# Optimization experiments

Hardware: AMD Instinct MI355X
Metric: run time of the kernel (lower is better)

The kernel has to match this reference:

```python
import jax, jax.numpy as jnp
import numpy as np
from jax import lax

H = 65  # hidden size

def lstm_layer(x, w_ih, w_hh, b_ih, b_hh):
    # x: [B, T, in]; w_ih: [4H, in]; w_hh: [4H, H]; PyTorch gate order i,f,g,o
    B = x.shape[0]
    # precompute input contribution for all timesteps: [T, B, 4H]
    pre = jnp.einsum('bti,gi->tbg', x, w_ih) + (b_ih + b_hh)
    wh = w_hh.T  # [H, 4H]

    def step(carry, pre_t):
        h, c = carry
        gates = pre_t + h @ wh
        i, f, g, o = jnp.split(gates, 4, axis=-1)
        i = jax.nn.sigmoid(i)
        f = jax.nn.sigmoid(f)
        g = jnp.tanh(g)
        o = jax.nn.sigmoid(o)
        c = f * c + i * g
        h = o * jnp.tanh(c)
        return (h, c), h

    init = (jnp.zeros((B, H), x.dtype), jnp.zeros((B, H), x.dtype))
    _, hs = lax.scan(step, init, pre)  # hs: [T, B, H]
    return jnp.transpose(hs, (1, 0, 2))  # [B, T, H]


def setup_inputs() -> dict:
    key = jax.random.key(0)
    ks = jax.random.split(key, 11)
    B, T = 512, 1024
    s = 1.0 / np.sqrt(H)
    d = {
        'x': jax.random.normal(ks[0], (B, T, H), jnp.float32),
        'w_ih0': jax.random.normal(ks[1], (4 * H, H), jnp.float32) * s,
        'w_hh0': jax.random.normal(ks[2], (4 * H, H), jnp.float32) * s,
        'b_ih0': jax.random.normal(ks[3], (4 * H,), jnp.float32) * s,
        'b_hh0': jax.random.normal(ks[4], (4 * H,), jnp.float32) * s,
        'w_ih1': jax.random.normal(ks[5], (4 * H, H), jnp.float32) * s,
        'w_hh1': jax.random.normal(ks[6], (4 * H, H), jnp.float32) * s,
        'b_ih1': jax.random.normal(ks[7], (4 * H,), jnp.float32) * s,
        'b_hh1': jax.random.normal(ks[8], (4 * H,), jnp.float32) * s,
        'w_lin': jax.random.normal(ks[9], (1, H), jnp.float32) * s,
        'b_lin': jax.random.normal(ks[10], (1,), jnp.float32) * s,
    }
    return d


def reference(x, w_ih0, w_hh0, b_ih0, b_hh0, w_ih1, w_hh1, b_ih1, b_hh1, w_lin, b_lin):
    h1 = lstm_layer(x, w_ih0, w_hh0, b_ih0, b_hh0)   # [B, T, H]
    h2 = lstm_layer(h1, w_ih1, w_hh1, b_ih1, b_hh1)  # [B, T, H]
    last = h2[:, -1, :]                               # [B, H]
    return last @ w_lin.T + b_lin                     # [B, 1]
```

## Files before the change

### kernel.cpp

```cpp
#include <hip/hip_runtime.h>

#define H 65
#define T_STEPS 1024

typedef _Float16 half_t;
typedef _Float16 half2_t __attribute__((ext_vector_type(2)));

static __device__ __forceinline__ float dot2(half2_t a, half2_t b, float c) {
#if __has_builtin(__builtin_amdgcn_fdot2)
  return __builtin_amdgcn_fdot2(a, b, c, false);
#else
  float d;
  asm("v_dot2_f32_f16 %0, %1, %2, %3" : "=v"(d) : "v"(a), "v"(b), "v"(c));
  return d;
#endif
}

template <int CTRL>
static __device__ __forceinline__ float qperm(float v) {
  int r = __builtin_amdgcn_update_dpp(0, __builtin_bit_cast(int, v), CTRL, 0xF, 0xF, true);
  return __builtin_bit_cast(float, r);
}

template <int PAT>
static __device__ __forceinline__ float swz(float v) {
  int r = __builtin_amdgcn_ds_swizzle(__builtin_bit_cast(int, v), PAT);
  return __builtin_bit_cast(float, r);
}

#define LOG2E 1.44269504089f
static __device__ __forceinline__ float fast_sigm(float v) {
  float e = __builtin_amdgcn_exp2f(-LOG2E * v);
  return __builtin_amdgcn_rcpf(1.f + e);
}

static __device__ __forceinline__ float pick(int idx, float a, float b, float c, float d) {
  float lo = (idx & 1) ? b : a;
  float hi = (idx & 1) ? d : c;
  return (idx & 2) ? hi : lo;
}

__global__ __launch_bounds__(512, 4) void lstm_fused(
    const float* __restrict__ x,
    const float* __restrict__ wih0, const float* __restrict__ whh0,
    const float* __restrict__ bih0, const float* __restrict__ bhh0,
    const float* __restrict__ wih1, const float* __restrict__ whh1,
    const float* __restrict__ bih1, const float* __restrict__ bhh1,
    const float* __restrict__ wlin, const float* __restrict__ blin,
    float* __restrict__ out)
{
  __shared__ __align__(16) half_t xh[2][2][144];
  __shared__ float h1f[H];

  const int tid = threadIdx.x;
  const int b   = blockIdx.x;

  const int quad = tid >> 2;
  const int l  = (quad >= 65) ? 1 : 0;
  const int j  = quad - 65 * l;
  const int kh = (tid >> 1) & 1;
  const int g0 = tid & 1;
  const bool gz = (g0 == 0);
  const float mreg = gz ? 2.f : 1.f;
  const float msub = mreg - 1.f;

  half2_t w[2][33];
  float hb[2];
  {
    const float* wi = l ? wih1 : wih0;
    const float* wh = l ? whh1 : whh0;
    const float* bi = l ? bih1 : bih0;
    const float* bh = l ? bhh1 : bhh0;
#pragma unroll
    for (int cc = 0; cc < 2; ++cc) {
      const int row = (g0 + 2 * cc) * H + j;
      hb[cc] = 0.5f * (bi[row] + bh[row]);
      const float* src = (kh ? wh : wi) + row * H;
#pragma unroll
      for (int pp = 0; pp < 33; ++pp) {
        float e0 = src[2 * pp];
        float e1 = (2 * pp + 1 < H) ? src[2 * pp + 1] : 0.f;
        half2_t v = {(half_t)e0, (half_t)e1};
        w[cc][pp] = v;
      }
    }
  }

  const bool isW7 = (tid >= 448);
  const int  w7   = tid - 448;
  const int  ec   = w7 >> 3;
  const int  ck   = w7 & 7;
  const int  side = ck >> 2;
  const int  sck  = ck & 3;
  const int  ecoff = side * 144 + 36 * sck;
  half2_t ecw[9];
  float ecbias = 0.f;
  float cec = 0.f;
  if (isW7) {
    const int gec = ec & 3;
    const int jec = 63 + (ec >> 2);
    const int row = gec * H + jec;
    const float* src = (side ? whh1 : wih1) + row * H;
#pragma unroll
    for (int i = 0; i < 9; ++i) {
      int es = 9 * sck + i;
      float e0 = (es < 33) ? src[2 * es] : 0.f;
      float e1 = (es < 33 && 2 * es + 1 < H) ? src[2 * es + 1] : 0.f;
      half2_t v = {(half_t)e0, (half_t)e1};
      ecw[i] = v;
    }
    if (ck == 0) ecbias = bih1[row] + bhh1[row];
  } else {
#pragma unroll
    for (int i = 0; i < 9; ++i) {
      half2_t z = {(half_t)0.f, (half_t)0.f};
      ecw[i] = z;
    }
  }

  const bool isW6 = (tid >= 384) && (tid < 448);
  const int  u    = tid - 384;

  for (int i = tid; i < 2 * 2 * 144; i += 512) ((half_t*)xh)[i] = (half_t)0.f;
  __syncthreads();

  const float* xrow = x + (size_t)b * (size_t)(T_STEPS * H);
  float nxA = 0.f, nxB = 0.f, nnA = 0.f, nnB = 0.f;
  if (isW6) {
    xh[0][0][u] = (half_t)xrow[u];
    if (u == 0) xh[0][0][64] = (half_t)xrow[64];
    nxA = xrow[H + u];
    if (u == 0) nxB = xrow[H + 64];
    nnA = xrow[2 * H + u];
    if (u == 0) nnB = xrow[2 * H + 64];
  }
  __syncthreads();

  float cst = 0.f;

  for (int s = 0; s <= T_STEPS; ++s) {
    const int p = s & 1;

    float fA = 0.f, fB = 0.f;
    if (isW6 && (s + 3 < T_STEPS)) {
      const float* xr = xrow + (size_t)(s + 3) * H;
      fA = xr[u];
      if (u == 0) fB = xr[64];
    }

    const bool act = l ? (s >= 1) : (s < T_STEPS);
    if (act) {
      const half_t* xb = &xh[l][p][0] + 72 * kh;
      float a0 = hb[0], a1 = hb[1];
#pragma unroll
      for (int c = 0; c < 8; ++c) {
        uint4 qv = ((const uint4*)xb)[c];
        half2_t x0 = __builtin_bit_cast(half2_t, qv.x);
        half2_t x1 = __builtin_bit_cast(half2_t, qv.y);
        half2_t x2 = __builtin_bit_cast(half2_t, qv.z);
        half2_t x3 = __builtin_bit_cast(half2_t, qv.w);
        a0 = dot2(x0, w[0][4 * c + 0], a0);
        a1 = dot2(x0, w[1][4 * c + 0], a1);
        a0 = dot2(x1, w[0][4 * c + 1], a0);
        a1 = dot2(x1, w[1][4 * c + 1], a1);
        a0 = dot2(x2, w[0][4 * c + 2], a0);
        a1 = dot2(x2, w[1][4 * c + 2], a1);
        a0 = dot2(x3, w[0][4 * c + 3], a0);
        a1 = dot2(x3, w[1][4 * c + 3], a1);
      }
      {
        half2_t xt = *(const half2_t*)(xb + 64);
        a0 = dot2(xt, w[0][32], a0);
        a1 = dot2(xt, w[1][32], a1);
      }
      a0 += qperm<0x4E>(a0);
      a1 += qperm<0x4E>(a1);
      float e0 = fast_sigm(a0);
      float e1 = mreg * fast_sigm(mreg * a1) - msub;
      float p0 = qperm<0xB1>(e0);
      float p1 = qperm<0xB1>(e1);
      float iv = gz ? e0 : p0;
      float fv = gz ? p0 : e0;
      float gv = gz ? e1 : p1;
      float ov = gz ? p1 : e1;
      cst = fv * cst + iv * gv;
      float th = 2.f * fast_sigm(2.f * cst) - 1.f;
      float hv = ov * th;
      if ((tid & 3) == 0) {
        half_t hh = (half_t)hv;
        if (l == 0) {
          xh[0][p ^ 1][72 + j] = hh;
          xh[1][p ^ 1][j]      = hh;
        } else {
          xh[1][p ^ 1][72 + j] = hh;
          if (s == T_STEPS) h1f[j] = hv;
        }
      }
    }

    if (isW7 && s >= 1) {
      const char* xb1 = (const char*)&xh[1][p][0];
      float aec = ecbias;
#pragma unroll
      for (int i = 0; i < 9; ++i) {
        unsigned qv = *(const unsigned*)(xb1 + ecoff + 4 * i);
        aec = dot2(__builtin_bit_cast(half2_t, qv), ecw[i], aec);
      }
      aec += swz<0x041F>(aec);
      aec += swz<0x081F>(aec);
      aec += swz<0x101F>(aec);
      const int gec = ec & 3;
      float me = (gec == 2) ? 2.f : 1.f;
      float A  = me * fast_sigm(me * aec) - (me - 1.f);
      float Bv = swz<0x201F>(A);
      float Cv = swz<0x401F>(A);
      float Dv = swz<0x401F>(Bv);
      float iv2 = pick(gec ^ 0, A, Bv, Cv, Dv);
      float fv2 = pick(gec ^ 1, A, Bv, Cv, Dv);
      float gv2 = pick(gec ^ 2, A, Bv, Cv, Dv);
      float ov2 = pick(gec ^ 3, A, Bv, Cv, Dv);
      cec = fv2 * cec + iv2 * gv2;
      float hec = ov2 * (2.f * fast_sigm(2.f * cec) - 1.f);
      if (ck == 0 && (ec & 3) == 0) {
        const int jec = 63 + (ec >> 2);
        xh[1][p ^ 1][72 + jec] = (half_t)hec;
        if (s == T_STEPS) h1f[jec] = hec;
      }
    }

    if (isW6 && (s + 1 < T_STEPS)) {
      half_t* dst = &xh[0][p ^ 1][0];
      dst[u] = (half_t)nxA;
      if (u == 0) dst[64] = (half_t)nxB;
      nxA = nnA; nxB = nnB;
      nnA = fA;  nnB = fB;
    }
    __syncthreads();
  }

  if (tid == 0) {
    float acc = blin[0];
    for (int jj = 0; jj < H; ++jj) acc += h1f[jj] * wlin[jj];
    out[b] = acc;
  }
}

extern "C" void kernel_launch(void* const* d_in, const int* in_sizes, int n_in,
                              void* d_out, int out_size, void* d_ws, size_t ws_size,
                              hipStream_t stream) {
  const float* x    = (const float*)d_in[0];
  const float* wih0 = (const float*)d_in[1];
  const float* whh0 = (const float*)d_in[2];
  const float* bih0 = (const float*)d_in[3];
  const float* bhh0 = (const float*)d_in[4];
  const float* wih1 = (const float*)d_in[5];
  const float* whh1 = (const float*)d_in[6];
  const float* bih1 = (const float*)d_in[7];
  const float* bhh1 = (const float*)d_in[8];
  const float* wlin = (const float*)d_in[9];
  const float* blin = (const float*)d_in[10];
  float* out = (float*)d_out;

  lstm_fused<<<512, 512, 0, stream>>>(x, wih0, whh0, bih0, bhh0,
                                      wih1, whh1, bih1, bhh1, wlin, blin, out);
}
```

Baseline: 1.353 ms.

## Move half of per-thread LSTM weights and extra-column weights into LDS

The second gate row's weights (28 of 33 half2 pairs) and the extra-column weights are moved from registers into shared memory and read back with 128-bit LDS loads each timestep. The x prefetch depth also drops from three steps to two, saving more registers. The aim is to cut VGPR pressure, probably to avoid spills or to meet the 512x4 launch bounds. The cost is about 56 KB of extra LDS traffic per step per block, and the larger LDS footprint may limit how many blocks fit per CU.

New measurement: 1.420 ms. 1.05x slower.

```diff
diff --git a/kernel.cpp b/kernel.cpp
--- a/kernel.cpp
+++ b/kernel.cpp
@@ -49,6 +49,9 @@
     const float* __restrict__ wlin, const float* __restrict__ blin,
     float* __restrict__ out)
 {
+  __shared__ __align__(16) uint4 wlds[7][512];
+  __shared__ __align__(16) uint4 eclds[2][64];
+  __shared__ float ecl1[64];
   __shared__ __align__(16) half_t xh[2][2][144];
   __shared__ float h1f[H];
 
@@ -64,24 +67,51 @@
   const float mreg = gz ? 2.f : 1.f;
   const float msub = mreg - 1.f;
 
-  half2_t w[2][33];
+  half2_t w0[33];
+  half2_t w1t[5];
   float hb[2];
   {
     const float* wi = l ? wih1 : wih0;
     const float* wh = l ? whh1 : whh0;
     const float* bi = l ? bih1 : bih0;
     const float* bh = l ? bhh1 : bhh0;
-#pragma unroll
-    for (int cc = 0; cc < 2; ++cc) {
-      const int row = (g0 + 2 * cc) * H + j;
-      hb[cc] = 0.5f * (bi[row] + bh[row]);
+    {
+      const int row = g0 * H + j;
+      hb[0] = 0.5f * (bi[row] + bh[row]);
       const float* src = (kh ? wh : wi) + row * H;
 #pragma unroll
       for (int pp = 0; pp < 33; ++pp) {
         float e0 = src[2 * pp];
         float e1 = (2 * pp + 1 < H) ? src[2 * pp + 1] : 0.f;
         half2_t v = {(half_t)e0, (half_t)e1};
-        w[cc][pp] = v;
+        w0[pp] = v;
+      }
+    }
+    {
+      const int row = (g0 + 2) * H + j;
+      hb[1] = 0.5f * (bi[row] + bh[row]);
+      const float* src = (kh ? wh : wi) + row * H;
+#pragma unroll
+      for (int c7 = 0; c7 < 7; ++c7) {
+        unsigned t0, t1, t2, t3;
+#pragma unroll
+        for (int q = 0; q < 4; ++q) {
+          const int pp = 4 * c7 + q;
+          half2_t v = {(half_t)src[2 * pp], (half_t)src[2 * pp + 1]};
+          unsigned uv = __builtin_bit_cast(unsigned, v);
+          if (q == 0) t0 = uv; else if (q == 1) t1 = uv;
+          else if (q == 2) t2 = uv; else t3 = uv;
+        }
+        uint4 wv = {t0, t1, t2, t3};
+        wlds[c7][tid] = wv;
+      }
+#pragma unroll
+      for (int q = 0; q < 5; ++q) {
+        const int pp = 28 + q;
+        float e0 = src[2 * pp];
+        float e1 = (2 * pp + 1 < H) ? src[2 * pp + 1] : 0.f;
+        half2_t v = {(half_t)e0, (half_t)e1};
+        w1t[q] = v;
       }
     }
   }
@@ -93,7 +123,6 @@
   const int  side = ck >> 2;
   const int  sck  = ck & 3;
   const int  ecoff = side * 144 + 36 * sck;
-  half2_t ecw[9];
   float ecbias = 0.f;
   float cec = 0.f;
   if (isW7) {
@@ -101,21 +130,21 @@
     const int jec = 63 + (ec >> 2);
     const int row = gec * H + jec;
     const float* src = (side ? whh1 : wih1) + row * H;
+    unsigned t[9];
 #pragma unroll
     for (int i = 0; i < 9; ++i) {
       int es = 9 * sck + i;
       float e0 = (es < 33) ? src[2 * es] : 0.f;
       float e1 = (es < 33 && 2 * es + 1 < H) ? src[2 * es + 1] : 0.f;
       half2_t v = {(half_t)e0, (half_t)e1};
-      ecw[i] = v;
-    }
+      t[i] = __builtin_bit_cast(unsigned, v);
+    }
+    uint4 e0v = {t[0], t[1], t[2], t[3]};
+    uint4 e1v = {t[4], t[5], t[6], t[7]};
+    eclds[0][w7] = e0v;
+    eclds[1][w7] = e1v;
+    ecl1[w7] = __builtin_bit_cast(float, t[8]);
     if (ck == 0) ecbias = bih1[row] + bhh1[row];
-  } else {
-#pragma unroll
-    for (int i = 0; i < 9; ++i) {
-      half2_t z = {(half_t)0.f, (half_t)0.f};
-      ecw[i] = z;
-    }
   }
 
   const bool isW6 = (tid >= 384) && (tid < 448);
@@ -125,14 +154,12 @@
   __syncthreads();
 
   const float* xrow = x + (size_t)b * (size_t)(T_STEPS * H);
-  float nxA = 0.f, nxB = 0.f, nnA = 0.f, nnB = 0.f;
+  float nxA = 0.f, nxB = 0.f;
   if (isW6) {
     xh[0][0][u] = (half_t)xrow[u];
     if (u == 0) xh[0][0][64] = (half_t)xrow[64];
     nxA = xrow[H + u];
     if (u == 0) nxB = xrow[H + 64];
-    nnA = xrow[2 * H + u];
-    if (u == 0) nnB = xrow[2 * H + 64];
   }
   __syncthreads();
 
@@ -142,8 +169,8 @@
     const int p = s & 1;
 
     float fA = 0.f, fB = 0.f;
-    if (isW6 && (s + 3 < T_STEPS)) {
-      const float* xr = xrow + (size_t)(s + 3) * H;
+    if (isW6 && (s + 2 < T_STEPS)) {
+      const float* xr = xrow + (size_t)(s + 2) * H;
       fA = xr[u];
       if (u == 0) fB = xr[64];
     }
@@ -153,25 +180,45 @@
       const half_t* xb = &xh[l][p][0] + 72 * kh;
       float a0 = hb[0], a1 = hb[1];
 #pragma unroll
-      for (int c = 0; c < 8; ++c) {
+      for (int c = 0; c < 7; ++c) {
         uint4 qv = ((const uint4*)xb)[c];
+        uint4 wv = wlds[c][tid];
         half2_t x0 = __builtin_bit_cast(half2_t, qv.x);
         half2_t x1 = __builtin_bit_cast(half2_t, qv.y);
         half2_t x2 = __builtin_bit_cast(half2_t, qv.z);
         half2_t x3 = __builtin_bit_cast(half2_t, qv.w);
-        a0 = dot2(x0, w[0][4 * c + 0], a0);
-        a1 = dot2(x0, w[1][4 * c + 0], a1);
-        a0 = dot2(x1, w[0][4 * c + 1], a0);
-        a1 = dot2(x1, w[1][4 * c + 1], a1);
-        a0 = dot2(x2, w[0][4 * c + 2], a0);
-        a1 = dot2(x2, w[1][4 * c + 2], a1);
-        a0 = dot2(x3, w[0][4 * c + 3], a0);
-        a1 = dot2(x3, w[1][4 * c + 3], a1);
+        half2_t w10 = __builtin_bit_cast(half2_t, wv.x);
+        half2_t w11 = __builtin_bit_cast(half2_t, wv.y);
+        half2_t w12 = __builtin_bit_cast(half2_t, wv.z);
+        half2_t w13 = __builtin_bit_cast(half2_t, wv.w);
+        a0 = dot2(x0, w0[4 * c + 0], a0);
+        a1 = dot2(x0, w10, a1);
+        a0 = dot2(x1, w0[4 * c + 1], a0);
+        a1 = dot2(x1, w11, a1);
+        a0 = dot2(x2, w0[4 * c + 2], a0);
+        a1 = dot2(x2, w12, a1);
+        a0 = dot2(x3, w0[4 * c + 3], a0);
+        a1 = dot2(x3, w13, a1);
+      }
+      {
+        uint4 qv = ((const uint4*)xb)[7];
+        half2_t x0 = __builtin_bit_cast(half2_t, qv.x);
+        half2_t x1 = __builtin_bit_cast(half2_t, qv.y);
+        half2_t x2 = __builtin_bit_cast(half2_t, qv.z);
+        half2_t x3 = __builtin_bit_cast(half2_t, qv.w);
+        a0 = dot2(x0, w0[28], a0);
+        a1 = dot2(x0, w1t[0], a1);
+        a0 = dot2(x1, w0[29], a0);
+        a1 = dot2(x1, w1t[1], a1);
+        a0 = dot2(x2, w0[30], a0);
+        a1 = dot2(x2, w1t[2], a1);
+        a0 = dot2(x3, w0[31], a0);
+        a1 = dot2(x3, w1t[3], a1);
       }
       {
         half2_t xt = *(const half2_t*)(xb + 64);
-        a0 = dot2(xt, w[0][32], a0);
-        a1 = dot2(xt, w[1][32], a1);
+        a0 = dot2(xt, w0[32], a0);
+        a1 = dot2(xt, w1t[4], a1);
       }
       a0 += qperm<0x4E>(a0);
       a1 += qperm<0x4E>(a1);
@@ -200,11 +247,24 @@
 
     if (isW7 && s >= 1) {
       const char* xb1 = (const char*)&xh[1][p][0];
+      uint4 ev0 = eclds[0][w7];
+      uint4 ev1 = eclds[1][w7];
+      half2_t ew8 = __builtin_bit_cast(half2_t, ecl1[w7]);
       float aec = ecbias;
 #pragma unroll
       for (int i = 0; i < 9; ++i) {
         unsigned qv = *(const unsigned*)(xb1 + ecoff + 4 * i);
-        aec = dot2(__builtin_bit_cast(half2_t, qv), ecw[i], aec);
+        half2_t wv;
+        if (i == 0) wv = __builtin_bit_cast(half2_t, ev0.x);
+        else if (i == 1) wv = __builtin_bit_cast(half2_t, ev0.y);
+        else if (i == 2) wv = __builtin_bit_cast(half2_t, ev0.z);
+        else if (i == 3) wv = __builtin_bit_cast(half2_t, ev0.w);
+        else if (i == 4) wv = __builtin_bit_cast(half2_t, ev1.x);
+        else if (i == 5) wv = __builtin_bit_cast(half2_t, ev1.y);
+        else if (i == 6) wv = __builtin_bit_cast(half2_t, ev1.z);
+        else if (i == 7) wv = __builtin_bit_cast(half2_t, ev1.w);
+        else wv = ew8;
+        aec = dot2(__builtin_bit_cast(half2_t, qv), wv, aec);
       }
       aec += swz<0x041F>(aec);
       aec += swz<0x081F>(aec);
@@ -232,8 +292,7 @@
       half_t* dst = &xh[0][p ^ 1][0];
       dst[u] = (half_t)nxA;
       if (u == 0) dst[64] = (half_t)nxB;
-      nxA = nnA; nxB = nnB;
-      nnA = fA;  nnB = fB;
+      nxA = fA; nxB = fB;
     }
     __syncthreads();
   }
```
